# Optimization experiments

Hardware: AMD Instinct MI355X
Metric: run time of the kernel (lower is better)

Reference implementation:

```python
import jax, jax.numpy as jnp
import numpy as np

B, T, D, L, N_MELS, MAX_R = 128, 1024, 256, 512, 80, 20

def setup_inputs() -> dict:
    key = jax.random.key(0)
    ks = jax.random.split(key, 40)
    s = 0.05
    inp = {
        'encoder_seq': jax.random.normal(ks[0], (B, T, D), jnp.float32),
        'encoder_seq_proj': jax.random.normal(ks[1], (B, T, D), jnp.float32),
        'prenet_in': jax.random.normal(ks[2], (B, N_MELS), jnp.float32),
        'attn_hidden': jax.random.normal(ks[3], (B, D), jnp.float32),
        'rnn1_hidden': jax.random.normal(ks[4], (B, L), jnp.float32),
        'rnn2_hidden': jax.random.normal(ks[5], (B, L), jnp.float32),
        'rnn1_cell': jax.random.normal(ks[6], (B, L), jnp.float32),
        'rnn2_cell': jax.random.normal(ks[7], (B, L), jnp.float32),
        'context_vec': jax.random.normal(ks[8], (B, D), jnp.float32),
        # PreNet
        'fc1_W': jax.random.normal(ks[9], (256, N_MELS), jnp.float32) * s,
        'fc1_b': jnp.zeros((256,), jnp.float32),
        'fc2_W': jax.random.normal(ks[10], (128, 256), jnp.float32) * s,
        'fc2_b': jnp.zeros((128,), jnp.float32),
        # Attention
        'attn_W': jax.random.normal(ks[11], (D, D), jnp.float32) * s,
        'attn_v': jax.random.normal(ks[12], (1, D), jnp.float32) * s,
        # GRUCell: input size D + D//2 = 384
        'gru_Wih': jax.random.normal(ks[13], (3 * D, D + D // 2), jnp.float32) * s,
        'gru_Whh': jax.random.normal(ks[14], (3 * D, D), jnp.float32) * s,
        'gru_bih': jnp.zeros((3 * D,), jnp.float32),
        'gru_bhh': jnp.zeros((3 * D,), jnp.float32),
        # rnn_input Linear: 2*D -> L
        'rnn_in_W': jax.random.normal(ks[15], (L, 2 * D), jnp.float32) * s,
        'rnn_in_b': jnp.zeros((L,), jnp.float32),
        # LSTMCell 1
        'l1_Wih': jax.random.normal(ks[16], (4 * L, L), jnp.float32) * s,
        'l1_Whh': jax.random.normal(ks[17], (4 * L, L), jnp.float32) * s,
        'l1_bih': jnp.zeros((4 * L,), jnp.float32),
        'l1_bhh': jnp.zeros((4 * L,), jnp.float32),
        # LSTMCell 2
        'l2_Wih': jax.random.normal(ks[18], (4 * L, L), jnp.float32) * s,
        'l2_Whh': jax.random.normal(ks[19], (4 * L, L), jnp.float32) * s,
        'l2_bih': jnp.zeros((4 * L,), jnp.float32),
        'l2_bhh': jnp.zeros((4 * L,), jnp.float32),
        # mel projection (no bias)
        'mel_W': jax.random.normal(ks[20], (N_MELS * MAX_R, L), jnp.float32) * s,
        'r': 2,
    }
    return inp


def _lstm_cell(x, h, c, Wih, Whh, bih, bhh):
    g = x @ Wih.T + bih + h @ Whh.T + bhh
    i, f, gg, o = jnp.split(g, 4, axis=-1)
    c_new = jax.nn.sigmoid(f) * c + jax.nn.sigmoid(i) * jnp.tanh(gg)
    h_new = jax.nn.sigmoid(o) * jnp.tanh(c_new)
    return h_new, c_new


def reference(encoder_seq, encoder_seq_proj, prenet_in, attn_hidden, rnn1_hidden,
              rnn2_hidden, rnn1_cell, rnn2_cell, context_vec,
              fc1_W, fc1_b, fc2_W, fc2_b, attn_W, attn_v,
              gru_Wih, gru_Whh, gru_bih, gru_bhh, rnn_in_W, rnn_in_b,
              l1_Wih, l1_Whh, l1_bih, l1_bhh, l2_Wih, l2_Whh, l2_bih, l2_bhh,
              mel_W, r):
    # PreNet (eval mode: dropout identity)
    p = jax.nn.relu(prenet_in @ fc1_W.T + fc1_b)
    p = jax.nn.relu(p @ fc2_W.T + fc2_b)  # [B, D//2]

    # GRUCell (torch semantics)
    x_in = jnp.concatenate([context_vec, p], axis=-1)  # [B, D + D//2]
    gi = x_in @ gru_Wih.T + gru_bih
    gh = attn_hidden @ gru_Whh.T + gru_bhh
    i_r, i_z, i_n = jnp.split(gi, 3, axis=-1)
    h_r, h_z, h_n = jnp.split(gh, 3, axis=-1)
    rg = jax.nn.sigmoid(i_r + h_r)
    zg = jax.nn.sigmoid(i_z + h_z)
    ng = jnp.tanh(i_n + rg * h_n)
    attn_h = (1.0 - zg) * ng + zg * attn_hidden  # [B, D]

    # Bahdanau attention, softmax over time (dim=1)
    q = attn_h @ attn_W.T  # [B, D]
    u = jnp.tanh(encoder_seq_proj + q[:, None, :]) @ attn_v.T  # [B, T, 1]
    scores = jax.nn.softmax(u, axis=1)
    scores_t = jnp.swapaxes(scores, 1, 2)  # [B, 1, T]
    context = jnp.matmul(scores_t, encoder_seq)[:, 0, :]  # [B, D]

    x = jnp.concatenate([context, attn_h], axis=1) @ rnn_in_W.T + rnn_in_b  # [B, L]

    rnn1_h, rnn1_c = _lstm_cell(x, rnn1_hidden, rnn1_cell, l1_Wih, l1_Whh, l1_bih, l1_bhh)
    x = x + rnn1_h
    rnn2_h, rnn2_c = _lstm_cell(x, rnn2_hidden, rnn2_cell, l2_Wih, l2_Whh, l2_bih, l2_bhh)
    x = x + rnn2_h

    mels = (x @ mel_W.T).reshape(x.shape[0], N_MELS, MAX_R)[:, :, :r]
    return (mels, scores_t, attn_h, rnn1_h, rnn2_h, rnn1_c, rnn2_c, context)
```

## Files before the change

kernel.cpp:

```cpp
#include <hip/hip_runtime.h>
#include <math.h>

#define B_   128
#define T_   1024
#define D_   256
#define L_   512

__device__ __forceinline__ float sigmoidf_(float x) {
    return 1.f / (1.f + __expf(-x));
}
__device__ __forceinline__ float tanhf_(float x) {
    x = fminf(fmaxf(x, -15.f), 15.f);
    float e = __expf(2.f * x);
    return (e - 1.f) / (e + 1.f);
}
__device__ __forceinline__ float tanh_fast(float x) {
    float e = __expf(2.f * x);
    return 1.f - 2.f * __builtin_amdgcn_rcpf(e + 1.f);
}
__device__ __forceinline__ float waveReduceSum(float v) {
    #pragma unroll
    for (int o = 32; o > 0; o >>= 1) v += __shfl_xor(v, o, 64);
    return v;
}

__global__ __launch_bounds__(256) void k1a_prenet(
    const float* __restrict__ prenet_in,
    const float* __restrict__ fc1_W, const float* __restrict__ fc1_b,
    const float* __restrict__ fc2_W, const float* __restrict__ fc2_b,
    float* __restrict__ p2_out)
{
    const int b = blockIdx.x, t = threadIdx.x;
    __shared__ __align__(16) float pin[80];
    __shared__ __align__(16) float p1[256];

    if (t < 80) pin[t] = prenet_in[b * 80 + t];
    __syncthreads();

    {
        float a = fc1_b[t];
        const float4* w  = (const float4*)(fc1_W + t * 80);
        const float4* xv = (const float4*)pin;
        #pragma unroll
        for (int k = 0; k < 20; k++) {
            float4 wv = w[k], v = xv[k];
            a += v.x * wv.x + v.y * wv.y + v.z * wv.z + v.w * wv.w;
        }
        p1[t] = fmaxf(a, 0.f);
    }
    __syncthreads();

    if (t < 128) {
        float a = fc2_b[t];
        const float4* w  = (const float4*)(fc2_W + t * 256);
        const float4* xv = (const float4*)p1;
        #pragma unroll 8
        for (int k = 0; k < 64; k++) {
            float4 wv = w[k], v = xv[k];
            a += v.x * wv.x + v.y * wv.y + v.z * wv.z + v.w * wv.w;
        }
        p2_out[b * 128 + t] = fmaxf(a, 0.f);
    }
}

__global__ __launch_bounds__(256) void k1b_gru_gemv(
    const float* __restrict__ context_vec, const float* __restrict__ p2,
    const float* __restrict__ attn_hidden,
    const float* __restrict__ gru_Wih, const float* __restrict__ gru_Whh,
    const float* __restrict__ gru_bih, const float* __restrict__ gru_bhh,
    float* __restrict__ gi_out, float* __restrict__ gh_out)
{
    const int t = threadIdx.x;
    const int j = blockIdx.x * 256 + t;
    const int b0 = blockIdx.y * 2;

    __shared__ __align__(16) float xs[2][384];
    __shared__ __align__(16) float hs[2][256];

    for (int i = t; i < 768; i += 256) {
        int bb = i / 384, k = i % 384;
        xs[bb][k] = (k < 256) ? context_vec[(b0 + bb) * 256 + k]
                              : p2[(b0 + bb) * 128 + (k - 256)];
    }
    for (int i = t; i < 512; i += 256) {
        hs[i / 256][i % 256] = attn_hidden[(b0 + i / 256) * 256 + (i % 256)];
    }
    __syncthreads();

    {
        float a0 = gru_bih[j], a1 = a0;
        const float4* w  = (const float4*)(gru_Wih + (size_t)j * 384);
        const float4* x0 = (const float4*)xs[0];
        const float4* x1 = (const float4*)xs[1];
        #pragma unroll 8
        for (int k = 0; k < 96; k++) {
            float4 wv = w[k], v0 = x0[k], v1 = x1[k];
            a0 += v0.x * wv.x + v0.y * wv.y + v0.z * wv.z + v0.w * wv.w;
            a1 += v1.x * wv.x + v1.y * wv.y + v1.z * wv.z + v1.w * wv.w;
        }
        gi_out[(size_t)(b0 + 0) * 768 + j] = a0;
        gi_out[(size_t)(b0 + 1) * 768 + j] = a1;
    }
    {
        float a0 = gru_bhh[j], a1 = a0;
        const float4* w  = (const float4*)(gru_Whh + (size_t)j * 256);
        const float4* x0 = (const float4*)hs[0];
        const float4* x1 = (const float4*)hs[1];
        #pragma unroll 8
        for (int k = 0; k < 64; k++) {
            float4 wv = w[k], v0 = x0[k], v1 = x1[k];
            a0 += v0.x * wv.x + v0.y * wv.y + v0.z * wv.z + v0.w * wv.w;
            a1 += v1.x * wv.x + v1.y * wv.y + v1.z * wv.z + v1.w * wv.w;
        }
        gh_out[(size_t)(b0 + 0) * 768 + j] = a0;
        gh_out[(size_t)(b0 + 1) * 768 + j] = a1;
    }
}

__global__ __launch_bounds__(256) void k1c_gates_q(
    const float* __restrict__ gi, const float* __restrict__ gh,
    const float* __restrict__ attn_hidden, const float* __restrict__ attn_W,
    float* __restrict__ attn_h_out, float* __restrict__ q_out)
{
    const int b = blockIdx.x, t = threadIdx.x;
    __shared__ __align__(16) float ahn[256];

    {
        float hp = attn_hidden[b * 256 + t];
        float rg = sigmoidf_(gi[(size_t)b * 768 + t]       + gh[(size_t)b * 768 + t]);
        float zg = sigmoidf_(gi[(size_t)b * 768 + 256 + t] + gh[(size_t)b * 768 + 256 + t]);
        float ng = tanhf_(gi[(size_t)b * 768 + 512 + t] + rg * gh[(size_t)b * 768 + 512 + t]);
        float h  = (1.f - zg) * ng + zg * hp;
        ahn[t] = h;
        attn_h_out[b * 256 + t] = h;
    }
    __syncthreads();

    {
        float a = 0.f;
        const float4* w  = (const float4*)(attn_W + (size_t)t * 256);
        const float4* xv = (const float4*)ahn;
        #pragma unroll 8
        for (int k = 0; k < 64; k++) {
            float4 wv = w[k], v = xv[k];
            a += v.x * wv.x + v.y * wv.y + v.z * wv.z + v.w * wv.w;
        }
        q_out[b * 256 + t] = a;
    }
}

__global__ __launch_bounds__(64) void ka_attn(
    const float* __restrict__ enc_proj, const float* __restrict__ enc,
    const float* __restrict__ q, const float* __restrict__ v,
    float* __restrict__ u_out, float* __restrict__ ctx_part,
    float* __restrict__ s_part)
{
    const int b     = blockIdx.x >> 4;
    const int chunk = blockIdx.x & 15;
    const int lane  = threadIdx.x;
    const int t0    = chunk * 64;

    __shared__ float lds_p[64][65];
    __shared__ __align__(16) float el[64];

    const float4 q4 = ((const float4*)(q + b * 256))[lane];
    const float4 v4 = ((const float4*)v)[lane];

    const float4* prow = (const float4*)(enc_proj + ((size_t)(b * T_ + t0)) * 256);
    #pragma unroll 8
    for (int r = 0; r < 64; r++) {
        float4 p = prow[(size_t)r * 64 + lane];
        float partial = tanh_fast(p.x + q4.x) * v4.x
                      + tanh_fast(p.y + q4.y) * v4.y
                      + tanh_fast(p.z + q4.z) * v4.z
                      + tanh_fast(p.w + q4.w) * v4.w;
        lds_p[r][lane] = partial;
    }
    __syncthreads();

    float u0 = 0.f, u1 = 0.f, u2 = 0.f, u3 = 0.f;
    #pragma unroll
    for (int j = 0; j < 64; j += 4) {
        u0 += lds_p[lane][j + 0];
        u1 += lds_p[lane][j + 1];
        u2 += lds_p[lane][j + 2];
        u3 += lds_p[lane][j + 3];
    }
    float u = (u0 + u1) + (u2 + u3);
    u_out[b * T_ + t0 + lane] = u;

    float e = __expf(u);
    el[lane] = e;
    float ssum = waveReduceSum(e);
    if (lane == 0) s_part[b * 16 + chunk] = ssum;
    __syncthreads();

    const float4* erow = (const float4*)(enc + ((size_t)(b * T_ + t0)) * 256);
    const float4* e4p  = (const float4*)el;
    float4 accA = {0.f, 0.f, 0.f, 0.f}, accB = {0.f, 0.f, 0.f, 0.f};

    #pragma unroll 4
    for (int t = 0; t < 64; t += 4) {
        float4 e4 = e4p[t >> 2];
        float4 r0 = erow[(size_t)(t + 0) * 64 + lane];
        float4 r1 = erow[(size_t)(t + 1) * 64 + lane];
        float4 r2 = erow[(size_t)(t + 2) * 64 + lane];
        float4 r3 = erow[(size_t)(t + 3) * 64 + lane];
        accA.x += e4.x * r0.x; accA.y += e4.x * r0.y; accA.z += e4.x * r0.z; accA.w += e4.x * r0.w;
        accB.x += e4.y * r1.x; accB.y += e4.y * r1.y; accB.z += e4.y * r1.z; accB.w += e4.y * r1.w;
        accA.x += e4.z * r2.x; accA.y += e4.z * r2.y; accA.z += e4.z * r2.z; accA.w += e4.z * r2.w;
        accB.x += e4.w * r3.x; accB.y += e4.w * r3.y; accB.z += e4.w * r3.z; accB.w += e4.w * r3.w;
    }
    accA.x += accB.x; accA.y += accB.y; accA.z += accB.z; accA.w += accB.w;
    ((float4*)ctx_part)[(size_t)(b * 16 + chunk) * 64 + lane] = accA;
}

__global__ __launch_bounds__(256) void kb_combine(
    const float* __restrict__ u, const float* __restrict__ s_part,
    const float* __restrict__ ctx_part, const float* __restrict__ attn_h,
    float* __restrict__ scores_out, float* __restrict__ ctx_out,
    float* __restrict__ concat1)
{
    const int b = blockIdx.x, tid = threadIdx.x;
    __shared__ float ssh[16];
    if (tid < 16) ssh[tid] = s_part[b * 16 + tid];
    __syncthreads();

    float S = 0.f;
    #pragma unroll
    for (int c = 0; c < 16; c++) S += ssh[c];
    float invS = 1.f / S;

    {
        float a = 0.f;
        #pragma unroll
        for (int c = 0; c < 16; c++)
            a += ctx_part[(size_t)(b * 16 + c) * 256 + tid];
        a *= invS;
        ctx_out[b * 256 + tid] = a;
        concat1[b * 512 + tid] = a;
        concat1[b * 512 + 256 + tid] = attn_h[b * 256 + tid];
    }

    #pragma unroll
    for (int i = 0; i < 4; i++) {
        int t = i * 256 + tid;
        scores_out[b * T_ + t] = __expf(u[b * T_ + t]) * invS;
    }
}

__global__ __launch_bounds__(256) void gemm512_splitk(
    const float* __restrict__ A1, const float* __restrict__ W1,
    const float* __restrict__ A2, const float* __restrict__ W2,
    float* __restrict__ part, int N, int ksPerSeg)
{
    const int n0 = blockIdx.x * 64, m0 = blockIdx.y * 64;
    const int seg = blockIdx.z / ksPerSeg, ls = blockIdx.z % ksPerSeg;
    const int KSZ = 512 / ksPerSeg;
    const float* A = seg ? A2 : A1;
    const float* W = seg ? W2 : W1;
    const int k0 = ls * KSZ;

    __shared__ __align__(16) float As[32][68];
    __shared__ __align__(16) float Ws[32][68];

    const int tid = threadIdx.x;
    const int tm = tid & 15, tn = tid >> 4;
    const int rs = tid >> 3, qs = tid & 7;

    float acc[4][4] = {};

    for (int kt = 0; kt < KSZ; kt += 32) {
        #pragma unroll
        for (int it = 0; it < 2; it++) {
            int r = rs + it * 32;
            float4 av = *(const float4*)(A + (size_t)(m0 + r) * 512 + k0 + kt + qs * 4);
            As[qs * 4 + 0][r] = av.x; As[qs * 4 + 1][r] = av.y;
            As[qs * 4 + 2][r] = av.z; As[qs * 4 + 3][r] = av.w;
            float4 wv = *(const float4*)(W + (size_t)(n0 + r) * 512 + k0 + kt + qs * 4);
            Ws[qs * 4 + 0][r] = wv.x; Ws[qs * 4 + 1][r] = wv.y;
            Ws[qs * 4 + 2][r] = wv.z; Ws[qs * 4 + 3][r] = wv.w;
        }
        __syncthreads();
        #pragma unroll
        for (int kk = 0; kk < 32; kk++) {
            float4 a = *(const float4*)&As[kk][tm * 4];
            float4 w = *(const float4*)&Ws[kk][tn * 4];
            acc[0][0] += a.x * w.x; acc[0][1] += a.x * w.y; acc[0][2] += a.x * w.z; acc[0][3] += a.x * w.w;
            acc[1][0] += a.y * w.x; acc[1][1] += a.y * w.y; acc[1][2] += a.y * w.z; acc[1][3] += a.y * w.w;
            acc[2][0] += a.z * w.x; acc[2][1] += a.z * w.y; acc[2][2] += a.z * w.z; acc[2][3] += a.z * w.w;
            acc[3][0] += a.w * w.x; acc[3][1] += a.w * w.y; acc[3][2] += a.w * w.z; acc[3][3] += a.w * w.w;
        }
        __syncthreads();
    }

    float* pb = part + ((size_t)blockIdx.z * 128 + m0) * N + n0;
    #pragma unroll
    for (int i = 0; i < 4; i++) {
        float4 o = {acc[i][0], acc[i][1], acc[i][2], acc[i][3]};
        *(float4*)(pb + (size_t)(tm * 4 + i) * N + tn * 4) = o;
    }
}

__global__ __launch_bounds__(256) void e_rnn(
    const float* __restrict__ part, const float* __restrict__ bias,
    float* __restrict__ x)
{
    const int idx = blockIdx.x * 256 + threadIdx.x;
    const int n = idx & 511;
    float a = bias[n];
    #pragma unroll
    for (int z = 0; z < 4; z++) a += part[(size_t)z * 65536 + idx];
    x[idx] = a;
}

__global__ __launch_bounds__(256) void e_lstm(
    const float* __restrict__ part,
    const float* __restrict__ bih, const float* __restrict__ bhh,
    const float* __restrict__ c_prev, const float* __restrict__ x_prev,
    float* __restrict__ h_out, float* __restrict__ c_out, float* __restrict__ x_new)
{
    const int idx = blockIdx.x * 256 + threadIdx.x;
    const int bb = idx >> 9, j = idx & 511;
    float gi = bih[j] + bhh[j];
    float gf = bih[512 + j] + bhh[512 + j];
    float gg = bih[1024 + j] + bhh[1024 + j];
    float go = bih[1536 + j] + bhh[1536 + j];
    #pragma unroll
    for (int z = 0; z < 4; z++) {
        const float* p = part + ((size_t)z * 128 + bb) * 2048;
        gi += p[j]; gf += p[512 + j]; gg += p[1024 + j]; go += p[1536 + j];
    }
    float c = sigmoidf_(gf) * c_prev[idx] + sigmoidf_(gi) * tanhf_(gg);
    float h = sigmoidf_(go) * tanhf_(c);
    h_out[idx] = h;
    c_out[idx] = c;
    x_new[idx] = x_prev[idx] + h;
}

__global__ __launch_bounds__(512) void e_lstm2_mel(
    const float* __restrict__ part,
    const float* __restrict__ bih, const float* __restrict__ bhh,
    const float* __restrict__ c_prev, const float* __restrict__ x_prev,
    const float* __restrict__ mel_W, const int* __restrict__ r_ptr,
    float* __restrict__ h_out, float* __restrict__ c_out,
    float* __restrict__ mels)
{
    const int b = blockIdx.x, j = threadIdx.x;
    __shared__ __align__(16) float xs[512];

    const int idx = b * 512 + j;
    float gi = bih[j] + bhh[j];
    float gf = bih[512 + j] + bhh[512 + j];
    float gg = bih[1024 + j] + bhh[1024 + j];
    float go = bih[1536 + j] + bhh[1536 + j];
    #pragma unroll
    for (int z = 0; z < 4; z++) {
        const float* p = part + ((size_t)z * 128 + b) * 2048;
        gi += p[j]; gf += p[512 + j]; gg += p[1024 + j]; go += p[1536 + j];
    }
    float c = sigmoidf_(gf) * c_prev[idx] + sigmoidf_(gi) * tanhf_(gg);
    float h = sigmoidf_(go) * tanhf_(c);
    h_out[idx] = h;
    c_out[idx] = c;
    xs[j] = x_prev[idx] + h;
    __syncthreads();

    const int r = r_ptr[0];
    const int tot = 80 * r;
    for (int n = j; n < tot; n += 512) {
        int m = n / r, rr = n % r;
        const float4* w  = (const float4*)(mel_W + (size_t)(m * 20 + rr) * 512);
        const float4* xv = (const float4*)xs;
        float a = 0.f;
        #pragma unroll 8
        for (int k = 0; k < 128; k++) {
            float4 wv = w[k], vv = xv[k];
            a += wv.x * vv.x + wv.y * vv.y + wv.z * vv.z + wv.w * vv.w;
        }
        mels[(size_t)b * tot + n] = a;
    }
}

extern "C" void kernel_launch(void* const* d_in, const int* in_sizes, int n_in,
                              void* d_out, int out_size, void* d_ws, size_t ws_size,
                              hipStream_t stream)
{
    const float* enc   = (const float*)d_in[0];
    const float* encp  = (const float*)d_in[1];
    const float* pre   = (const float*)d_in[2];
    const float* ah_in = (const float*)d_in[3];
    const float* r1h   = (const float*)d_in[4];
    const float* r2h   = (const float*)d_in[5];
    const float* r1c   = (const float*)d_in[6];
    const float* r2c   = (const float*)d_in[7];
    const float* cvec  = (const float*)d_in[8];
    const float* fc1W  = (const float*)d_in[9];
    const float* fc1b  = (const float*)d_in[10];
    const float* fc2W  = (const float*)d_in[11];
    const float* fc2b  = (const float*)d_in[12];
    const float* attnW = (const float*)d_in[13];
    const float* attnv = (const float*)d_in[14];
    const float* gWih  = (const float*)d_in[15];
    const float* gWhh  = (const float*)d_in[16];
    const float* gbih  = (const float*)d_in[17];
    const float* gbhh  = (const float*)d_in[18];
    const float* rinW  = (const float*)d_in[19];
    const float* rinb  = (const float*)d_in[20];
    const float* l1Wih = (const float*)d_in[21];
    const float* l1Whh = (const float*)d_in[22];
    const float* l1bih = (const float*)d_in[23];
    const float* l1bhh = (const float*)d_in[24];
    const float* l2Wih = (const float*)d_in[25];
    const float* l2Whh = (const float*)d_in[26];
    const float* l2bih = (const float*)d_in[27];
    const float* l2bhh = (const float*)d_in[28];
    const float* melW  = (const float*)d_in[29];
    const int*   rp    = (const int*)d_in[30];

    float* out = (float*)d_out;
    float* o_mels  = out + 0;
    float* o_scor  = out + 20480;
    float* o_attnh = out + 151552;
    float* o_r1h   = out + 184320;
    float* o_r2h   = out + 249856;
    float* o_r1c   = out + 315392;
    float* o_r2c   = out + 380928;
    float* o_ctx   = out + 446464;

    float* ws     = (float*)d_ws;
    float* w_q    = ws + 0;
    float* w_u    = ws + 32768;
    float* w_s    = ws + 163840;
    float* w_ctxp = ws + 165888;
    float* w_cat1 = ws + 692224;
    float* w_x    = ws + 757760;
    float* w_x2   = ws + 823296;
    float* w_part = ws + 888832;

    float* w_p2 = w_part;
    float* w_gi = w_part + 16384;
    float* w_gh = w_part + 114688;

    hipLaunchKernelGGL(k1a_prenet, dim3(128), dim3(256), 0, stream,
                       pre, fc1W, fc1b, fc2W, fc2b, w_p2);

    hipLaunchKernelGGL(k1b_gru_gemv, dim3(3, 64), dim3(256), 0, stream,
                       cvec, w_p2, ah_in, gWih, gWhh, gbih, gbhh, w_gi, w_gh);

    hipLaunchKernelGGL(k1c_gates_q, dim3(128), dim3(256), 0, stream,
                       w_gi, w_gh, ah_in, attnW, o_attnh, w_q);

    hipLaunchKernelGGL(ka_attn, dim3(2048), dim3(64), 0, stream,
                       encp, enc, w_q, attnv, w_u, w_ctxp, w_s);

    hipLaunchKernelGGL(kb_combine, dim3(128), dim3(256), 0, stream,
                       w_u, w_s, w_ctxp, o_attnh, o_scor, o_ctx, w_cat1);

    hipLaunchKernelGGL(gemm512_splitk, dim3(8, 2, 4), dim3(256), 0, stream,
                       w_cat1, rinW, w_cat1, rinW, w_part, 512, 4);
    hipLaunchKernelGGL(e_rnn, dim3(256), dim3(256), 0, stream, w_part, rinb, w_x);

    hipLaunchKernelGGL(gemm512_splitk, dim3(32, 2, 4), dim3(256), 0, stream,
                       w_x, l1Wih, r1h, l1Whh, w_part, 2048, 2);
    hipLaunchKernelGGL(e_lstm, dim3(256), dim3(256), 0, stream,
                       w_part, l1bih, l1bhh, r1c, w_x, o_r1h, o_r1c, w_x2);

    hipLaunchKernelGGL(gemm512_splitk, dim3(32, 2, 4), dim3(256), 0, stream,
                       w_x2, l2Wih, r2h, l2Whh, w_part, 2048, 2);
    hipLaunchKernelGGL(e_lstm2_mel, dim3(128), dim3(512), 0, stream,
                       w_part, l2bih, l2bhh, r2c, w_x2, melW, rp,
                       o_r2h, o_r2c, o_mels);
}
```

Before: 154.0 us.

## Split attention into separate score and context kernels; raise split-K for rnn_in GEMM

The fused single-wave attention kernel is split into two 256-thread kernels. One computes the tanh scores over 32-row slabs per wave, and the other recomputes exp(u), accumulates the weighted encoder rows across four waves, and reduces them in LDS. The intent is more waves per block and more occupancy on the memory-bound encoder passes. The price is an extra launch and a round trip of u through global memory. Separately, the rnn_in GEMM split-K goes from 4 to 16 so the small GEMM fills more CUs, with e_rnn summing 16 partials; this assumes the partial buffer is large enough to hold them.

```diff
diff --git a/kernel.cpp b/kernel.cpp
--- a/kernel.cpp
+++ b/kernel.cpp
@@ -149,70 +149,90 @@
     }
 }
 
-__global__ __launch_bounds__(64) void ka_attn(
-    const float* __restrict__ enc_proj, const float* __restrict__ enc,
-    const float* __restrict__ q, const float* __restrict__ v,
-    float* __restrict__ u_out, float* __restrict__ ctx_part,
-    float* __restrict__ s_part)
+__global__ __launch_bounds__(256, 4) void ku_scores(
+    const float* __restrict__ enc_proj, const float* __restrict__ q,
+    const float* __restrict__ v, float* __restrict__ u_out)
+{
+    const int b    = blockIdx.x >> 3;
+    const int slab = blockIdx.x & 7;
+    const int tid  = threadIdx.x;
+    const int wv   = tid >> 6, lane = tid & 63;
+    const int t0w  = slab * 128 + wv * 32;
+
+    __shared__ float lds_p[4][32][65];
+
+    const float4 q4 = ((const float4*)(q + b * 256))[lane];
+    const float4 v4 = ((const float4*)v)[lane];
+
+    const float4* prow = (const float4*)(enc_proj + ((size_t)(b * T_ + t0w)) * 256);
+    #pragma unroll 8
+    for (int r = 0; r < 32; r++) {
+        float4 p = prow[(size_t)r * 64 + lane];
+        lds_p[wv][r][lane] = tanh_fast(p.x + q4.x) * v4.x
+                           + tanh_fast(p.y + q4.y) * v4.y
+                           + tanh_fast(p.z + q4.z) * v4.z
+                           + tanh_fast(p.w + q4.w) * v4.w;
+    }
+
+    const int row = lane >> 1, half = lane & 1;
+    float u0 = 0.f, u1 = 0.f, u2 = 0.f, u3 = 0.f;
+    #pragma unroll
+    for (int j = 0; j < 32; j += 4) {
+        u0 += lds_p[wv][row][half * 32 + j + 0];
+        u1 += lds_p[wv][row][half * 32 + j + 1];
+        u2 += lds_p[wv][row][half * 32 + j + 2];
+        u3 += lds_p[wv][row][half * 32 + j + 3];
+    }
+    float us = (u0 + u1) + (u2 + u3);
+    us += __shfl_xor(us, 1, 64);
+    if (half == 0) u_out[b * T_ + t0w + row] = us;
+}
+
+__global__ __launch_bounds__(256, 4) void kc_context(
+    const float* __restrict__ enc, const float* __restrict__ u_in,
+    float* __restrict__ ctx_part, float* __restrict__ s_part)
 {
     const int b     = blockIdx.x >> 4;
     const int chunk = blockIdx.x & 15;
-    const int lane  = threadIdx.x;
+    const int tid   = threadIdx.x;
+    const int wv    = tid >> 6, lane = tid & 63;
     const int t0    = chunk * 64;
 
-    __shared__ float lds_p[64][65];
-    __shared__ __align__(16) float el[64];
-
-    const float4 q4 = ((const float4*)(q + b * 256))[lane];
-    const float4 v4 = ((const float4*)v)[lane];
-
-    const float4* prow = (const float4*)(enc_proj + ((size_t)(b * T_ + t0)) * 256);
-    #pragma unroll 8
-    for (int r = 0; r < 64; r++) {
-        float4 p = prow[(size_t)r * 64 + lane];
-        float partial = tanh_fast(p.x + q4.x) * v4.x
-                      + tanh_fast(p.y + q4.y) * v4.y
-                      + tanh_fast(p.z + q4.z) * v4.z
-                      + tanh_fast(p.w + q4.w) * v4.w;
-        lds_p[r][lane] = partial;
-    }
-    __syncthreads();
-
-    float u0 = 0.f, u1 = 0.f, u2 = 0.f, u3 = 0.f;
-    #pragma unroll
-    for (int j = 0; j < 64; j += 4) {
-        u0 += lds_p[lane][j + 0];
-        u1 += lds_p[lane][j + 1];
-        u2 += lds_p[lane][j + 2];
-        u3 += lds_p[lane][j + 3];
-    }
-    float u = (u0 + u1) + (u2 + u3);
-    u_out[b * T_ + t0 + lane] = u;
-
-    float e = __expf(u);
-    el[lane] = e;
-    float ssum = waveReduceSum(e);
-    if (lane == 0) s_part[b * 16 + chunk] = ssum;
-    __syncthreads();
-
-    const float4* erow = (const float4*)(enc + ((size_t)(b * T_ + t0)) * 256);
-    const float4* e4p  = (const float4*)el;
+    __shared__ __align__(16) float4 red[3][64];
+    __shared__ float sred[4];
+
+    const float* ub = u_in + b * T_ + t0 + wv * 16;
+    float e[16];
+    float ssum = 0.f;
+    #pragma unroll
+    for (int j = 0; j < 16; j++) { e[j] = __expf(ub[j]); ssum += e[j]; }
+    if (lane == 0) sred[wv] = ssum;
+
+    const float4* erow = (const float4*)(enc + ((size_t)(b * T_ + t0 + wv * 16)) * 256);
     float4 accA = {0.f, 0.f, 0.f, 0.f}, accB = {0.f, 0.f, 0.f, 0.f};
-
-    #pragma unroll 4
-    for (int t = 0; t < 64; t += 4) {
-        float4 e4 = e4p[t >> 2];
-        float4 r0 = erow[(size_t)(t + 0) * 64 + lane];
-        float4 r1 = erow[(size_t)(t + 1) * 64 + lane];
-        float4 r2 = erow[(size_t)(t + 2) * 64 + lane];
-        float4 r3 = erow[(size_t)(t + 3) * 64 + lane];
-        accA.x += e4.x * r0.x; accA.y += e4.x * r0.y; accA.z += e4.x * r0.z; accA.w += e4.x * r0.w;
-        accB.x += e4.y * r1.x; accB.y += e4.y * r1.y; accB.z += e4.y * r1.z; accB.w += e4.y * r1.w;
-        accA.x += e4.z * r2.x; accA.y += e4.z * r2.y; accA.z += e4.z * r2.z; accA.w += e4.z * r2.w;
-        accB.x += e4.w * r3.x; accB.y += e4.w * r3.y; accB.z += e4.w * r3.z; accB.w += e4.w * r3.w;
+    #pragma unroll
+    for (int j = 0; j < 16; j += 2) {
+        float4 r0 = erow[(size_t)(j + 0) * 64 + lane];
+        float4 r1 = erow[(size_t)(j + 1) * 64 + lane];
+        accA.x += e[j] * r0.x;     accA.y += e[j] * r0.y;
+        accA.z += e[j] * r0.z;     accA.w += e[j] * r0.w;
+        accB.x += e[j + 1] * r1.x; accB.y += e[j + 1] * r1.y;
+        accB.z += e[j + 1] * r1.z; accB.w += e[j + 1] * r1.w;
     }
     accA.x += accB.x; accA.y += accB.y; accA.z += accB.z; accA.w += accB.w;
-    ((float4*)ctx_part)[(size_t)(b * 16 + chunk) * 64 + lane] = accA;
+
+    if (wv) red[wv - 1][lane] = accA;
+    __syncthreads();
+    if (wv == 0) {
+        float4 a1 = red[0][lane], a2 = red[1][lane], a3 = red[2][lane];
+        accA.x += a1.x + a2.x + a3.x;
+        accA.y += a1.y + a2.y + a3.y;
+        accA.z += a1.z + a2.z + a3.z;
+        accA.w += a1.w + a2.w + a3.w;
+        ((float4*)ctx_part)[(size_t)(b * 16 + chunk) * 64 + lane] = accA;
+        if (lane == 0)
+            s_part[b * 16 + chunk] = sred[0] + sred[1] + sred[2] + sred[3];
+    }
 }
 
 __global__ __launch_bounds__(256) void kb_combine(
@@ -310,7 +330,7 @@
     const int n = idx & 511;
     float a = bias[n];
     #pragma unroll
-    for (int z = 0; z < 4; z++) a += part[(size_t)z * 65536 + idx];
+    for (int z = 0; z < 16; z++) a += part[(size_t)z * 65536 + idx];
     x[idx] = a;
 }
 
@@ -451,14 +471,17 @@
     hipLaunchKernelGGL(k1c_gates_q, dim3(128), dim3(256), 0, stream,
                        w_gi, w_gh, ah_in, attnW, o_attnh, w_q);
 
-    hipLaunchKernelGGL(ka_attn, dim3(2048), dim3(64), 0, stream,
-                       encp, enc, w_q, attnv, w_u, w_ctxp, w_s);
+    hipLaunchKernelGGL(ku_scores, dim3(1024), dim3(256), 0, stream,
+                       encp, w_q, attnv, w_u);
+
+    hipLaunchKernelGGL(kc_context, dim3(2048), dim3(256), 0, stream,
+                       enc, w_u, w_ctxp, w_s);
 
     hipLaunchKernelGGL(kb_combine, dim3(128), dim3(256), 0, stream,
                        w_u, w_s, w_ctxp, o_attnh, o_scor, o_ctx, w_cat1);
 
-    hipLaunchKernelGGL(gemm512_splitk, dim3(8, 2, 4), dim3(256), 0, stream,
-                       w_cat1, rinW, w_cat1, rinW, w_part, 512, 4);
+    hipLaunchKernelGGL(gemm512_splitk, dim3(8, 2, 16), dim3(256), 0, stream,
+                       w_cat1, rinW, w_cat1, rinW, w_part, 512, 16);
     hipLaunchKernelGGL(e_rnn, dim3(256), dim3(256), 0, stream, w_part, rinb, w_x);
 
     hipLaunchKernelGGL(gemm512_splitk, dim3(32, 2, 4), dim3(256), 0, stream,
```

After: 155.1 us. Within noise of the previous version (+0.7%).
